# Kernel tuning notes

Hardware: AMD Instinct MI355X
Metric: run time of the kernel (lower is better)

The kernel has to match this reference:

```python
import jax, jax.numpy as jnp
import numpy as np

N_NODES = 20000
N_EDGES = 320000
IN_DIM = 512
HID = 256
N_GRAPHS = 256


def setup_inputs() -> dict:
    key = jax.random.key(0)
    ks = jax.random.split(key, 7)
    x = jax.random.normal(ks[0], (N_NODES, IN_DIM), dtype=jnp.float32)
    edge_index = jax.random.randint(ks[1], (2, N_EDGES), 0, N_NODES, dtype=jnp.int64)
    batch = jnp.sort(jax.random.randint(ks[2], (N_NODES,), 0, N_GRAPHS, dtype=jnp.int64))
    W = jax.random.normal(ks[3], (IN_DIM, HID), dtype=jnp.float32) * (1.0 / np.sqrt(IN_DIM))
    b = jax.random.normal(ks[4], (HID,), dtype=jnp.float32) * 0.02
    lin_w = jax.random.normal(ks[5], (HID, 1), dtype=jnp.float32) * (1.0 / np.sqrt(HID))
    lin_b = jax.random.normal(ks[6], (1,), dtype=jnp.float32) * 0.02
    return {"x": x, "edge_index": edge_index, "batch": batch,
            "W": W, "b": b, "lin_w": lin_w, "lin_b": lin_b}


def reference(x, edge_index, batch, W, b, lin_w, lin_b):
    N = x.shape[0]
    # --- GCNConv: add self-loops, symmetric normalization ---
    loop = jnp.arange(N, dtype=edge_index.dtype)
    src = jnp.concatenate([edge_index[0], loop])   # [E+N]
    dst = jnp.concatenate([edge_index[1], loop])   # [E+N]
    deg = jax.ops.segment_sum(jnp.ones_like(dst, dtype=x.dtype), dst, num_segments=N)
    dinv = jnp.where(deg > 0, jax.lax.rsqrt(deg), 0.0)          # [N]
    norm = dinv[src] * dinv[dst]                                 # [E+N]
    h = x @ W                                                    # [N, HID] dense GEMM
    msgs = h[src] * norm[:, None]                                # gather + scale
    agg = jax.ops.segment_sum(msgs, dst, num_segments=N) + b     # scatter-add
    xr = jax.nn.relu(agg)                                        # [N, HID]
    # --- global_mean_pool over graph ids ---
    sums = jax.ops.segment_sum(xr, batch, num_segments=N_GRAPHS)             # [G, HID]
    counts = jax.ops.segment_sum(jnp.ones((N,), dtype=x.dtype), batch, num_segments=N_GRAPHS)
    pooled = sums / jnp.maximum(counts, 1.0)[:, None]
    # --- linear head + sigmoid ---
    out = jax.nn.sigmoid(pooled @ lin_w + lin_b)                 # [G, 1]
    return out.reshape(-1)
```

## Files before the change

### kernel.cpp

```cpp
#include <hip/hip_runtime.h>
#include <hip/hip_bf16.h>
#include <cstdint>

typedef __attribute__((ext_vector_type(8))) _Float16 half8;
typedef __attribute__((ext_vector_type(2))) float f32x2;
typedef __attribute__((ext_vector_type(4))) float f32x4;

#define N_NODES 20000
#define N_EDGES 320000
#define IN_DIM 512
#define HID 256
#define N_GRAPHS 256
#define NPB 8
#define ECH 1024

#define PREP_W   (IN_DIM * HID)
#define PREP_E   (PREP_W + N_EDGES)
#define PREP_B   (PREP_E + N_NODES)
__global__ __launch_bounds__(256) void prep_kernel(const float* __restrict__ W,
                                                   const int* __restrict__ dst,
                                                   const int* __restrict__ batch,
                                                   _Float16* __restrict__ wt,
                                                   int* __restrict__ ecnt,
                                                   int* __restrict__ counts) {
    int t = blockIdx.x * 256 + threadIdx.x;
    if (t < PREP_W) {
        wt[t] = (_Float16)W[(t & 511) * HID + (t >> 9)];
    } else if (t < PREP_E) {
        atomicAdd(&ecnt[dst[t - PREP_W]], 1);
    } else if (t < PREP_B) {
        atomicAdd(&counts[batch[t - PREP_E]], 1);
    }
}

__global__ __launch_bounds__(1024) void scan_dinv_kernel(const int* __restrict__ ecnt,
                                                         int* __restrict__ offsets,
                                                         float* __restrict__ dinv) {
    __shared__ int wsum[16];
    int t = threadIdx.x;
    int lane = t & 63, wid = t >> 6;
    const int CHS = 20;
    int base = t * CHS;
    int vals[CHS];
    int s = 0;
    if (t < 1000) {
        const int4* p = reinterpret_cast<const int4*>(ecnt + base);
#pragma unroll
        for (int i = 0; i < 5; ++i) {
            int4 v = p[i];
            vals[4*i+0] = v.x; vals[4*i+1] = v.y; vals[4*i+2] = v.z; vals[4*i+3] = v.w;
        }
#pragma unroll
        for (int i = 0; i < CHS; ++i) s += vals[i];
    }
    int incl = s;
#pragma unroll
    for (int off = 1; off < 64; off <<= 1) {
        int u = __shfl_up(incl, off, 64);
        if (lane >= off) incl += u;
    }
    if (lane == 63) wsum[wid] = incl;
    __syncthreads();
    if (t < 16) {
        int v = wsum[t];
#pragma unroll
        for (int off = 1; off < 16; off <<= 1) {
            int u = __shfl_up(v, off, 16);
            if (t >= off) v += u;
        }
        wsum[t] = v;
    }
    __syncthreads();
    int woff = (wid == 0) ? 0 : wsum[wid - 1];
    if (t < 1000) {
        int run = woff + incl - s;
#pragma unroll
        for (int i = 0; i < CHS; ++i) {
            int idx = base + i;
            offsets[idx] = run;
            dinv[idx] = rsqrtf((float)(vals[i] + 1));
            run += vals[i];
        }
    }
    if (t == 1023) offsets[N_NODES] = wsum[15];
}

#define GEMM_BLOCKS ((N_NODES + 63) / 64)
#define CSR_BLOCKS  ((N_EDGES + 255) / 256)
__global__ __launch_bounds__(256) void gemm_csr_kernel(const float* __restrict__ x,
                                                       const _Float16* __restrict__ wt,
                                                       unsigned char* __restrict__ h8,
                                                       const int* __restrict__ src,
                                                       const int* __restrict__ dst,
                                                       const float* __restrict__ dinv,
                                                       const int* __restrict__ offsets,
                                                       int* __restrict__ cnt2,
                                                       int2* __restrict__ csr) {
    __shared__ _Float16 bsl[16 * 16 * 32];
    if (blockIdx.x >= GEMM_BLOCKS) {
        int e = (blockIdx.x - GEMM_BLOCKS) * 256 + threadIdx.x;
        if (e < N_EDGES) {
            int s = src[e], d = dst[e];
            int slot = offsets[d] + atomicAdd(&cnt2[d], 1);
            int2 pk;
            pk.x = s;
            pk.y = __float_as_int(dinv[s] * dinv[d]);
            csr[slot] = pk;
        }
        return;
    }
    const int K = IN_DIM;
    int t    = threadIdx.x;
    int wave = t >> 6;
    int lane = t & 63;
    int col  = lane & 15;
    int quad = lane >> 4;
    int row0 = blockIdx.x * 64 + wave * 16;

    f32x4 acc[16];
#pragma unroll
    for (int i = 0; i < 16; ++i) acc[i] = (f32x4){0.f, 0.f, 0.f, 0.f};

    int arow = row0 + col;
    if (arow >= N_NODES) arow = N_NODES - 1;
    const float* aptr = x + (size_t)arow * K + quad * 8;
    const uint4* wsrc = reinterpret_cast<const uint4*>(wt + (size_t)t * K);

    float4 pa0 = *reinterpret_cast<const float4*>(aptr);
    float4 pa1 = *reinterpret_cast<const float4*>(aptr + 4);
    uint4 b0 = wsrc[0], b1 = wsrc[1], b2 = wsrc[2], b3 = wsrc[3];

    for (int k0 = 0; k0 < K; k0 += 32) {
        __syncthreads();
        {
            uint4* d = reinterpret_cast<uint4*>(&bsl[t * 32]);
            d[0] = b0; d[1] = b1; d[2] = b2; d[3] = b3;
        }
        __syncthreads();
        half8 a;
        a[0] = (_Float16)pa0.x; a[1] = (_Float16)pa0.y;
        a[2] = (_Float16)pa0.z; a[3] = (_Float16)pa0.w;
        a[4] = (_Float16)pa1.x; a[5] = (_Float16)pa1.y;
        a[6] = (_Float16)pa1.z; a[7] = (_Float16)pa1.w;
        if (k0 + 32 < K) {
            const float* ap = aptr + k0 + 32;
            pa0 = *reinterpret_cast<const float4*>(ap);
            pa1 = *reinterpret_cast<const float4*>(ap + 4);
            const uint4* ws = wsrc + ((k0 + 32) >> 3);
            b0 = ws[0]; b1 = ws[1]; b2 = ws[2]; b3 = ws[3];
        }
#pragma unroll
        for (int nt = 0; nt < 16; ++nt) {
            half8 b = *reinterpret_cast<const half8*>(&bsl[(nt * 16 + col) * 32 + quad * 8]);
            acc[nt] = __builtin_amdgcn_mfma_f32_16x16x32_f16(a, b, acc[nt], 0, 0, 0);
        }
    }

    int orow0 = row0 + quad * 4;
#pragma unroll
    for (int nt = 0; nt < 16; ++nt) {
#pragma unroll
        for (int r = 0; r < 4; ++r) {
            int rr = orow0 + r;
            if (rr < N_NODES) {
                int pk = __builtin_amdgcn_cvt_pk_fp8_f32(acc[nt][r], acc[nt][r], 0, false);
                h8[(size_t)rr * HID + nt * 16 + col] = (unsigned char)(pk & 0xff);
            }
        }
    }
}

__global__ __launch_bounds__(256, 8) void aggregate_kernel(const unsigned char* __restrict__ h8,
                                                           const float* __restrict__ bias,
                                                           const float* __restrict__ dinv,
                                                           const int* __restrict__ offsets,
                                                           const int2* __restrict__ csr,
                                                           const int* __restrict__ batch,
                                                           float* __restrict__ sums) {
    __shared__ int2 s_e[ECH];
    float* pool = reinterpret_cast<float*>(s_e);
    int v0  = blockIdx.x * NPB;
    int t   = threadIdx.x;
    int grp = t >> 6;
    int fl  = t & 63;
    int vg  = v0 + grp * 2;
    const float4 bf = *reinterpret_cast<const float4*>(bias + 4 * fl);

    int off[3];
#pragma unroll
    for (int i = 0; i <= 2; ++i) off[i] = offsets[vg + i];
    int beg0 = offsets[v0], end0 = offsets[v0 + NPB];

    float a0[2], a1[2], a2[2], a3[2];
#pragma unroll
    for (int i = 0; i < 2; ++i) {
        int v = vg + i;
        float dv = dinv[v];
        float d2 = dv * dv;
        unsigned int u = *reinterpret_cast<const unsigned int*>(h8 + (size_t)v * HID + 4 * fl);
        f32x2 lo = __builtin_amdgcn_cvt_pk_f32_fp8(u, false);
        f32x2 hi = __builtin_amdgcn_cvt_pk_f32_fp8(u, true);
        a0[i] = d2 * lo[0]; a1[i] = d2 * lo[1];
        a2[i] = d2 * hi[0]; a3[i] = d2 * hi[1];
    }

    for (int cb = beg0; cb < end0; cb += ECH) {
        int n = min(ECH, end0 - cb);
        for (int tt = t; tt < n; tt += 256) s_e[tt] = csr[cb + tt];
        __syncthreads();
#pragma unroll
        for (int i = 0; i < 2; ++i) {
            int lo_ = off[i] - cb;     if (lo_ < 0) lo_ = 0;
            int hi_ = off[i + 1] - cb; if (hi_ > n) hi_ = n;
            float x0 = a0[i], x1 = a1[i], x2 = a2[i], x3 = a3[i];
            int j = lo_;
            for (; j + 8 <= hi_; j += 8) {
#pragma unroll
                for (int q = 0; q < 8; ++q) {
                    int2 e = s_e[j + q];
                    unsigned int u = *reinterpret_cast<const unsigned int*>(
                        h8 + (size_t)e.x * HID + 4 * fl);
                    float w = __int_as_float(e.y);
                    f32x2 lo = __builtin_amdgcn_cvt_pk_f32_fp8(u, false);
                    f32x2 hi = __builtin_amdgcn_cvt_pk_f32_fp8(u, true);
                    x0 += w * lo[0]; x1 += w * lo[1];
                    x2 += w * hi[0]; x3 += w * hi[1];
                }
            }
            for (; j < hi_; ++j) {
                int2 e = s_e[j];
                unsigned int u = *reinterpret_cast<const unsigned int*>(
                    h8 + (size_t)e.x * HID + 4 * fl);
                float w = __int_as_float(e.y);
                f32x2 lo = __builtin_amdgcn_cvt_pk_f32_fp8(u, false);
                f32x2 hi = __builtin_amdgcn_cvt_pk_f32_fp8(u, true);
                x0 += w * lo[0]; x1 += w * lo[1];
                x2 += w * hi[0]; x3 += w * hi[1];
            }
            a0[i] = x0; a1[i] = x1; a2[i] = x2; a3[i] = x3;
        }
        __syncthreads();
    }

#pragma unroll
    for (int i = 0; i < 2; ++i) {
        f32x4 r;
        r[0] = fmaxf(a0[i] + bf.x, 0.f);
        r[1] = fmaxf(a1[i] + bf.y, 0.f);
        r[2] = fmaxf(a2[i] + bf.z, 0.f);
        r[3] = fmaxf(a3[i] + bf.w, 0.f);
        *reinterpret_cast<f32x4*>(&pool[(grp * 2 + i) * HID + 4 * fl]) = r;
    }
    __syncthreads();

    float acc = 0.f;
    int cur_g = batch[v0];
#pragma unroll
    for (int i = 0; i < NPB; ++i) {
        float val = pool[i * HID + t];
        int g = batch[v0 + i];
        if (g != cur_g) {
            atomicAdd(&sums[(size_t)cur_g * HID + t], acc);
            acc = 0.f;
            cur_g = g;
        }
        acc += val;
    }
    atomicAdd(&sums[(size_t)cur_g * HID + t], acc);
}

__global__ __launch_bounds__(256) void head_kernel(const float* __restrict__ sums,
                                                   const int* __restrict__ counts,
                                                   const float* __restrict__ lin_w,
                                                   const float* __restrict__ lin_b,
                                                   float* __restrict__ out) {
    int g = blockIdx.x;
    int f = threadIdx.x;
    float c = (float)counts[g];
    if (c < 1.f) c = 1.f;
    float v = (sums[(size_t)g * HID + f] / c) * lin_w[f];
#pragma unroll
    for (int off = 32; off >= 1; off >>= 1) v += __shfl_down(v, off, 64);
    __shared__ float red[4];
    if ((f & 63) == 0) red[f >> 6] = v;
    __syncthreads();
    if (f == 0) {
        float s = red[0] + red[1] + red[2] + red[3] + lin_b[0];
        out[g] = 1.0f / (1.0f + expf(-s));
    }
}

extern "C" void kernel_launch(void* const* d_in, const int* in_sizes, int n_in,
                              void* d_out, int out_size, void* d_ws, size_t ws_size,
                              hipStream_t stream) {
    const float* x     = (const float*)d_in[0];
    const int*   edge  = (const int*)d_in[1];
    const int*   batch = (const int*)d_in[2];
    const float* W     = (const float*)d_in[3];
    const float* b     = (const float*)d_in[4];
    const float* lin_w = (const float*)d_in[5];
    const float* lin_b = (const float*)d_in[6];
    float*       out   = (float*)d_out;

    const int N = N_NODES, E = N_EDGES, G = N_GRAPHS, K = IN_DIM, H = HID;
    const int* src = edge;
    const int* dst = edge + E;

    char* p = (char*)d_ws;
    auto alloc = [&](size_t bytes) {
        char* r = p;
        p += (bytes + 255) & ~(size_t)255;
        return r;
    };
    _Float16*      wt      = (_Float16*)alloc((size_t)H * K * 2);
    unsigned char* h8      = (unsigned char*)alloc((size_t)N * H);
    float*         dinv    = (float*)alloc((size_t)N * 4);
    int*           offsets = (int*)alloc((size_t)(N + 1) * 4);
    int2*          csr     = (int2*)alloc((size_t)E * 8);
    char* z0 = p;
    int*   ecnt   = (int*)alloc((size_t)N * 4);
    int*   cnt2   = (int*)alloc((size_t)N * 4);
    float* sums   = (float*)alloc((size_t)G * H * 4);
    int*   counts = (int*)alloc((size_t)G * 4);
    size_t zbytes = (size_t)(p - z0);

    hipMemsetAsync(z0, 0, zbytes, stream);

    prep_kernel<<<(PREP_B + 255) / 256, 256, 0, stream>>>(W, dst, batch, wt, ecnt, counts);
    scan_dinv_kernel<<<1, 1024, 0, stream>>>(ecnt, offsets, dinv);
    gemm_csr_kernel<<<GEMM_BLOCKS + CSR_BLOCKS, 256, 0, stream>>>(x, wt, h8, src, dst,
                                                                  dinv, offsets, cnt2, csr);
    aggregate_kernel<<<N / NPB, 256, 0, stream>>>(h8, b, dinv, offsets, csr, batch, sums);
    head_kernel<<<G, 256, 0, stream>>>(sums, counts, lin_w, lin_b, out);
}
```

Before: 189.5 us.

## Fold source normalization into GEMM output, shrink CSR, double-buffer GEMM LDS

The source-side dinv factor is multiplied into h before FP8 quantization, and the destination-side dinv is applied once after aggregation. This lets the CSR hold only source indices (4 bytes instead of 8) and removes the per-edge weight multiply in the gather loop. The GEMM now uses double-buffered, XOR-swizzled LDS for the weight tile, with one barrier per k-step instead of two. The weight transpose in prep goes through a shared-memory tile so the writes are coalesced, and the edge chunk size grows to 2048. Scaling by dinv before FP8 quantization changes the rounding error slightly.

```diff
diff --git a/kernel.cpp b/kernel.cpp
--- a/kernel.cpp
+++ b/kernel.cpp
@@ -3,6 +3,7 @@
 #include <cstdint>
 
 typedef __attribute__((ext_vector_type(8))) _Float16 half8;
+typedef __attribute__((ext_vector_type(4))) _Float16 half4;
 typedef __attribute__((ext_vector_type(2))) float f32x2;
 typedef __attribute__((ext_vector_type(4))) float f32x4;
 
@@ -12,24 +13,46 @@
 #define HID 256
 #define N_GRAPHS 256
 #define NPB 8
-#define ECH 1024
-
-#define PREP_W   (IN_DIM * HID)
-#define PREP_E   (PREP_W + N_EDGES)
-#define PREP_B   (PREP_E + N_NODES)
+#define ECH 2048
+
+#define PREP_WBLK 16
+#define PREP_EBLK (N_EDGES / 256)
+#define PREP_BBLK ((N_NODES + 255) / 256)
 __global__ __launch_bounds__(256) void prep_kernel(const float* __restrict__ W,
                                                    const int* __restrict__ dst,
                                                    const int* __restrict__ batch,
                                                    _Float16* __restrict__ wt,
                                                    int* __restrict__ ecnt,
                                                    int* __restrict__ counts) {
-    int t = blockIdx.x * 256 + threadIdx.x;
-    if (t < PREP_W) {
-        wt[t] = (_Float16)W[(t & 511) * HID + (t >> 9)];
-    } else if (t < PREP_E) {
-        atomicAdd(&ecnt[dst[t - PREP_W]], 1);
-    } else if (t < PREP_B) {
-        atomicAdd(&counts[batch[t - PREP_E]], 1);
+    int b = blockIdx.x, t = threadIdx.x;
+    if (b < PREP_WBLK) {
+        __shared__ _Float16 tile[32 * 256];
+        int k0 = b * 32;
+        const float4* wp = reinterpret_cast<const float4*>(W + (size_t)k0 * HID);
+#pragma unroll
+        for (int i = 0; i < 8; ++i) {
+            float4 v = wp[i * 256 + t];
+            int flat = (i * 256 + t) * 4;
+            int kk = flat >> 8, n = flat & 255;
+            half4 hv;
+            hv[0] = (_Float16)v.x; hv[1] = (_Float16)v.y;
+            hv[2] = (_Float16)v.z; hv[3] = (_Float16)v.w;
+            *reinterpret_cast<half4*>(&tile[kk * 256 + n]) = hv;
+        }
+        __syncthreads();
+        alignas(16) _Float16 vals[32];
+#pragma unroll
+        for (int kk = 0; kk < 32; ++kk) vals[kk] = tile[kk * 256 + t];
+        uint4* op = reinterpret_cast<uint4*>((char*)wt + (size_t)t * 1024 + (size_t)k0 * 2);
+        const uint4* vp = reinterpret_cast<const uint4*>(vals);
+#pragma unroll
+        for (int j = 0; j < 4; ++j) op[j] = vp[j];
+    } else if (b < PREP_WBLK + PREP_EBLK) {
+        int e = (b - PREP_WBLK) * 256 + t;
+        atomicAdd(&ecnt[dst[e]], 1);
+    } else {
+        int i = (b - PREP_WBLK - PREP_EBLK) * 256 + t;
+        if (i < N_NODES) atomicAdd(&counts[batch[i]], 1);
     }
 }
 
@@ -95,24 +118,21 @@
                                                        const float* __restrict__ dinv,
                                                        const int* __restrict__ offsets,
                                                        int* __restrict__ cnt2,
-                                                       int2* __restrict__ csr) {
-    __shared__ _Float16 bsl[16 * 16 * 32];
+                                                       int* __restrict__ csr) {
+    __shared__ _Float16 bsl[2 * 256 * 32];
     if (blockIdx.x >= GEMM_BLOCKS) {
         int e = (blockIdx.x - GEMM_BLOCKS) * 256 + threadIdx.x;
         if (e < N_EDGES) {
-            int s = src[e], d = dst[e];
+            int d = dst[e];
             int slot = offsets[d] + atomicAdd(&cnt2[d], 1);
-            int2 pk;
-            pk.x = s;
-            pk.y = __float_as_int(dinv[s] * dinv[d]);
-            csr[slot] = pk;
+            csr[slot] = src[e];
         }
         return;
     }
     const int K = IN_DIM;
     int t    = threadIdx.x;
+    int lane = t & 63;
     int wave = t >> 6;
-    int lane = t & 63;
     int col  = lane & 15;
     int quad = lane >> 4;
     int row0 = blockIdx.x * 64 + wave * 16;
@@ -130,13 +150,19 @@
     float4 pa1 = *reinterpret_cast<const float4*>(aptr + 4);
     uint4 b0 = wsrc[0], b1 = wsrc[1], b2 = wsrc[2], b3 = wsrc[3];
 
+    char* myst = (char*)bsl + t * 64;
+    int fsw = (t >> 1) & 3;
+    {
+        uint4* d = reinterpret_cast<uint4*>(myst);
+        d[0 ^ fsw] = b0; d[1 ^ fsw] = b1; d[2 ^ fsw] = b2; d[3 ^ fsw] = b3;
+    }
+    b0 = wsrc[4]; b1 = wsrc[5]; b2 = wsrc[6]; b3 = wsrc[7];
+    asm volatile("s_waitcnt lgkmcnt(0)" ::: "memory");
+    __builtin_amdgcn_s_barrier();
+    asm volatile("" ::: "memory");
+
+    int p = 0;
     for (int k0 = 0; k0 < K; k0 += 32) {
-        __syncthreads();
-        {
-            uint4* d = reinterpret_cast<uint4*>(&bsl[t * 32]);
-            d[0] = b0; d[1] = b1; d[2] = b2; d[3] = b3;
-        }
-        __syncthreads();
         half8 a;
         a[0] = (_Float16)pa0.x; a[1] = (_Float16)pa0.y;
         a[2] = (_Float16)pa0.z; a[3] = (_Float16)pa0.w;
@@ -146,24 +172,43 @@
             const float* ap = aptr + k0 + 32;
             pa0 = *reinterpret_cast<const float4*>(ap);
             pa1 = *reinterpret_cast<const float4*>(ap + 4);
-            const uint4* ws = wsrc + ((k0 + 32) >> 3);
-            b0 = ws[0]; b1 = ws[1]; b2 = ws[2]; b3 = ws[3];
-        }
+            uint4* d = reinterpret_cast<uint4*>(myst + ((p ^ 1) << 14));
+            d[0 ^ fsw] = b0; d[1 ^ fsw] = b1; d[2 ^ fsw] = b2; d[3 ^ fsw] = b3;
+            if (k0 + 64 < K) {
+                const uint4* ws = wsrc + ((k0 + 64) >> 3);
+                b0 = ws[0]; b1 = ws[1]; b2 = ws[2]; b3 = ws[3];
+            }
+        }
+        const char* rb = (const char*)bsl + (p << 14);
 #pragma unroll
         for (int nt = 0; nt < 16; ++nt) {
-            half8 b = *reinterpret_cast<const half8*>(&bsl[(nt * 16 + col) * 32 + quad * 8]);
-            acc[nt] = __builtin_amdgcn_mfma_f32_16x16x32_f16(a, b, acc[nt], 0, 0, 0);
-        }
+            int c = nt * 16 + col;
+            int fr = (c >> 1) & 3;
+            half8 bb = *reinterpret_cast<const half8*>(rb + c * 64 + ((quad ^ fr) << 4));
+            acc[nt] = __builtin_amdgcn_mfma_f32_16x16x32_f16(a, bb, acc[nt], 0, 0, 0);
+        }
+        asm volatile("s_waitcnt lgkmcnt(0)" ::: "memory");
+        __builtin_amdgcn_s_barrier();
+        asm volatile("" ::: "memory");
+        p ^= 1;
     }
 
     int orow0 = row0 + quad * 4;
+    float dv[4];
+#pragma unroll
+    for (int r = 0; r < 4; ++r) {
+        int rr = orow0 + r;
+        if (rr >= N_NODES) rr = N_NODES - 1;
+        dv[r] = dinv[rr];
+    }
 #pragma unroll
     for (int nt = 0; nt < 16; ++nt) {
 #pragma unroll
         for (int r = 0; r < 4; ++r) {
             int rr = orow0 + r;
             if (rr < N_NODES) {
-                int pk = __builtin_amdgcn_cvt_pk_fp8_f32(acc[nt][r], acc[nt][r], 0, false);
+                float v = acc[nt][r] * dv[r];
+                int pk = __builtin_amdgcn_cvt_pk_fp8_f32(v, v, 0, false);
                 h8[(size_t)rr * HID + nt * 16 + col] = (unsigned char)(pk & 0xff);
             }
         }
@@ -174,10 +219,10 @@
                                                            const float* __restrict__ bias,
                                                            const float* __restrict__ dinv,
                                                            const int* __restrict__ offsets,
-                                                           const int2* __restrict__ csr,
+                                                           const int* __restrict__ csr,
                                                            const int* __restrict__ batch,
                                                            float* __restrict__ sums) {
-    __shared__ int2 s_e[ECH];
+    __shared__ int s_e[ECH];
     float* pool = reinterpret_cast<float*>(s_e);
     int v0  = blockIdx.x * NPB;
     int t   = threadIdx.x;
@@ -191,17 +236,15 @@
     for (int i = 0; i <= 2; ++i) off[i] = offsets[vg + i];
     int beg0 = offsets[v0], end0 = offsets[v0 + NPB];
 
-    float a0[2], a1[2], a2[2], a3[2];
+    float a0[2], a1[2], a2[2], a3[2], dvv[2];
 #pragma unroll
     for (int i = 0; i < 2; ++i) {
         int v = vg + i;
-        float dv = dinv[v];
-        float d2 = dv * dv;
+        dvv[i] = dinv[v];
         unsigned int u = *reinterpret_cast<const unsigned int*>(h8 + (size_t)v * HID + 4 * fl);
         f32x2 lo = __builtin_amdgcn_cvt_pk_f32_fp8(u, false);
         f32x2 hi = __builtin_amdgcn_cvt_pk_f32_fp8(u, true);
-        a0[i] = d2 * lo[0]; a1[i] = d2 * lo[1];
-        a2[i] = d2 * hi[0]; a3[i] = d2 * hi[1];
+        a0[i] = lo[0]; a1[i] = lo[1]; a2[i] = hi[0]; a3[i] = hi[1];
     }
 
     for (int cb = beg0; cb < end0; cb += ECH) {
@@ -217,25 +260,23 @@
             for (; j + 8 <= hi_; j += 8) {
 #pragma unroll
                 for (int q = 0; q < 8; ++q) {
-                    int2 e = s_e[j + q];
+                    int s = s_e[j + q];
                     unsigned int u = *reinterpret_cast<const unsigned int*>(
-                        h8 + (size_t)e.x * HID + 4 * fl);
-                    float w = __int_as_float(e.y);
+                        h8 + (size_t)s * HID + 4 * fl);
                     f32x2 lo = __builtin_amdgcn_cvt_pk_f32_fp8(u, false);
                     f32x2 hi = __builtin_amdgcn_cvt_pk_f32_fp8(u, true);
-                    x0 += w * lo[0]; x1 += w * lo[1];
-                    x2 += w * hi[0]; x3 += w * hi[1];
+                    x0 += lo[0]; x1 += lo[1];
+                    x2 += hi[0]; x3 += hi[1];
                 }
             }
             for (; j < hi_; ++j) {
-                int2 e = s_e[j];
+                int s = s_e[j];
                 unsigned int u = *reinterpret_cast<const unsigned int*>(
-                    h8 + (size_t)e.x * HID + 4 * fl);
-                float w = __int_as_float(e.y);
+                    h8 + (size_t)s * HID + 4 * fl);
                 f32x2 lo = __builtin_amdgcn_cvt_pk_f32_fp8(u, false);
                 f32x2 hi = __builtin_amdgcn_cvt_pk_f32_fp8(u, true);
-                x0 += w * lo[0]; x1 += w * lo[1];
-                x2 += w * hi[0]; x3 += w * hi[1];
+                x0 += lo[0]; x1 += lo[1];
+                x2 += hi[0]; x3 += hi[1];
             }
             a0[i] = x0; a1[i] = x1; a2[i] = x2; a3[i] = x3;
         }
@@ -245,10 +286,10 @@
 #pragma unroll
     for (int i = 0; i < 2; ++i) {
         f32x4 r;
-        r[0] = fmaxf(a0[i] + bf.x, 0.f);
-        r[1] = fmaxf(a1[i] + bf.y, 0.f);
-        r[2] = fmaxf(a2[i] + bf.z, 0.f);
-        r[3] = fmaxf(a3[i] + bf.w, 0.f);
+        r[0] = fmaxf(dvv[i] * a0[i] + bf.x, 0.f);
+        r[1] = fmaxf(dvv[i] * a1[i] + bf.y, 0.f);
+        r[2] = fmaxf(dvv[i] * a2[i] + bf.z, 0.f);
+        r[3] = fmaxf(dvv[i] * a3[i] + bf.w, 0.f);
         *reinterpret_cast<f32x4*>(&pool[(grp * 2 + i) * HID + 4 * fl]) = r;
     }
     __syncthreads();
@@ -316,7 +357,7 @@
     unsigned char* h8      = (unsigned char*)alloc((size_t)N * H);
     float*         dinv    = (float*)alloc((size_t)N * 4);
     int*           offsets = (int*)alloc((size_t)(N + 1) * 4);
-    int2*          csr     = (int2*)alloc((size_t)E * 8);
+    int*           csr     = (int*)alloc((size_t)E * 4);
     char* z0 = p;
     int*   ecnt   = (int*)alloc((size_t)N * 4);
     int*   cnt2   = (int*)alloc((size_t)N * 4);
@@ -326,7 +367,8 @@
 
     hipMemsetAsync(z0, 0, zbytes, stream);
 
-    prep_kernel<<<(PREP_B + 255) / 256, 256, 0, stream>>>(W, dst, batch, wt, ecnt, counts);
+    prep_kernel<<<PREP_WBLK + PREP_EBLK + PREP_BBLK, 256, 0, stream>>>(W, dst, batch,
+                                                                       wt, ecnt, counts);
     scan_dinv_kernel<<<1, 1024, 0, stream>>>(ecnt, offsets, dinv);
     gemm_csr_kernel<<<GEMM_BLOCKS + CSR_BLOCKS, 256, 0, stream>>>(x, wt, h8, src, dst,
                                                                   dinv, offsets, cnt2, csr);
```

Measured after the change: 179.8 us. 5.1% less time.
